# Kernel optimization log

Hardware: AMD Instinct MI355X
Metric: run time of the kernel (lower is better)

The kernel has to match this reference:

```python
import jax, jax.numpy as jnp
import numpy as np

N, DH, DK, FF = 2048, 256, 64, 32


def setup_inputs() -> dict:
    key = jax.random.key(0)
    ks = jax.random.split(key, 12)
    s = lambda d: 1.0 / np.sqrt(d).astype(np.float32)
    return {
        "x": jax.random.normal(ks[0], (1, N, DH), dtype=jnp.float32),
        "adj": (jax.random.uniform(ks[1], (N, N)) < 0.05).astype(jnp.float32),
        "dense": jax.random.uniform(ks[2], (N, N), dtype=jnp.float32),
        "Wq": jax.random.normal(ks[3], (DH, DK)) * s(DH),
        "bq": jnp.zeros((DK,), jnp.float32),
        "Wk": jax.random.normal(ks[4], (DH, DK)) * s(DH),
        "bk": jnp.zeros((DK,), jnp.float32),
        "Wv": jax.random.normal(ks[5], (DH, DH)) * s(DH),
        "bv": jnp.zeros((DH,), jnp.float32),
        "W1": jax.random.normal(ks[6], (3, FF)) * s(3),
        "b1": jnp.zeros((FF,), jnp.float32),
        "W2": jax.random.normal(ks[7], (FF, FF)) * s(FF),
        "b2": jnp.zeros((FF,), jnp.float32),
        "W3": jax.random.normal(ks[8], (FF, 1)) * s(FF),
        "b3": jnp.zeros((1,), jnp.float32),
    }


def reference(x, adj, dense, Wq, bq, Wk, bk, Wv, bv, W1, b1, W2, b2, W3, b3):
    # x: (1, n, dh). Original repeats x to (n, n, dh); here we exploit that
    # q[i, j] = Q(x_j), k[i, j] = K(x_i), v[i, j] = V(x_j) so no n^2*dh tensor
    # is materialized, while the math is identical.
    x0 = x[0]                      # (n, dh)
    q = x0 @ Wq + bq               # (n, dk), Q(x_j)
    k = x0 @ Wk + bk               # (n, dk), K(x_i)
    v = x0 @ Wv + bv               # (n, dh), V(x_j)
    # out[i, j] = <Q(x_j), K(x_i)>
    scores = k @ q.T               # (n, n)
    feats = jnp.stack((scores, adj, dense), axis=2)      # (n, n, 3)
    h = jax.nn.relu(feats @ W1 + b1)                     # (n, n, FF)
    h = jax.nn.relu(h @ W2 + b2)                         # (n, n, FF)
    focus = jax.nn.softmax((h @ W3 + b3)[..., 0], axis=1)  # (n, n)
    # feature[i] = sum_j focus[i, j] * V(x_j)
    feature = focus @ v            # (n, dh)
    return feature[None]           # (1, n, dh)
```

## Files before the change

kernel.cpp:

```cpp
#include <hip/hip_runtime.h>
#include <math.h>


#define NN  2048
#define DHH 256
#define DKK 64

typedef float    f32x4 __attribute__((ext_vector_type(4)));
typedef _Float16 f16x8 __attribute__((ext_vector_type(8)));
typedef _Float16 f16x4 __attribute__((ext_vector_type(4)));
typedef _Float16 f16x2 __attribute__((ext_vector_type(2)));

__global__ __launch_bounds__(256) void k_qkv(
    const float* __restrict__ x,
    const float* __restrict__ Wq, const float* __restrict__ bq,
    const float* __restrict__ Wk, const float* __restrict__ bk,
    const float* __restrict__ Wv, const float* __restrict__ bv,
    _Float16* __restrict__ q16, _Float16* __restrict__ k16,
    _Float16* __restrict__ vT)
{
    __shared__ float As[32][64];
    __shared__ float Bs[32][64];
    __shared__ _Float16 Ts[64 * 72];

    const int t  = threadIdx.x;
    const int m0 = blockIdx.x * 64;
    const int yb = blockIdx.y;

    const float* W; const float* bias; int wld; int cw0;
    if (yb == 0)      { W = Wq; bias = bq; wld = 64;  cw0 = 0; }
    else if (yb == 1) { W = Wk; bias = bk; wld = 64;  cw0 = 0; }
    else              { W = Wv; bias = bv; wld = 256; cw0 = (yb - 2) * 64; }

    const int tx = t & 15, ty = t >> 4;
    float acc[4][4] = {};

    for (int k0 = 0; k0 < DHH; k0 += 32) {
        {
            const int rr = t >> 3;
            const int cc = (t & 7) * 4;
            float4 a0 = *(const float4*)(x + (size_t)(m0 + rr)      * DHH + k0 + cc);
            float4 a1 = *(const float4*)(x + (size_t)(m0 + rr + 32) * DHH + k0 + cc);
            As[cc+0][rr]    = a0.x; As[cc+1][rr]    = a0.y; As[cc+2][rr]    = a0.z; As[cc+3][rr]    = a0.w;
            As[cc+0][rr+32] = a1.x; As[cc+1][rr+32] = a1.y; As[cc+2][rr+32] = a1.z; As[cc+3][rr+32] = a1.w;
        }
        {
            const int bk_ = t >> 4;
            const int bc  = (t & 15) * 4;
            *(float4*)&Bs[bk_][bc]      = *(const float4*)(W + (size_t)(k0 + bk_)      * wld + cw0 + bc);
            *(float4*)&Bs[bk_ + 16][bc] = *(const float4*)(W + (size_t)(k0 + bk_ + 16) * wld + cw0 + bc);
        }
        __syncthreads();
        #pragma unroll
        for (int kk = 0; kk < 32; ++kk) {
            float4 a = *(const float4*)&As[kk][ty * 4];
            float4 b = *(const float4*)&Bs[kk][tx * 4];
            float av[4] = {a.x, a.y, a.z, a.w};
            float bw[4] = {b.x, b.y, b.z, b.w};
            #pragma unroll
            for (int ii = 0; ii < 4; ++ii)
                #pragma unroll
                for (int jj = 0; jj < 4; ++jj)
                    acc[ii][jj] = fmaf(av[ii], bw[jj], acc[ii][jj]);
        }
        __syncthreads();
    }

    float4 b4 = *(const float4*)&bias[cw0 + tx * 4];
    float bc4[4] = {b4.x, b4.y, b4.z, b4.w};

    if (yb < 2) {
        _Float16* outp = (yb == 0) ? q16 : k16;
        #pragma unroll
        for (int ii = 0; ii < 4; ++ii) {
            f16x4 hv;
            #pragma unroll
            for (int jj = 0; jj < 4; ++jj) hv[jj] = (_Float16)(acc[ii][jj] + bc4[jj]);
            *(f16x4*)&outp[(size_t)(m0 + ty * 4 + ii) * 64 + tx * 4] = hv;
        }
    } else {
        #pragma unroll
        for (int jj = 0; jj < 4; ++jj) {
            f16x4 hv;
            #pragma unroll
            for (int ii = 0; ii < 4; ++ii) hv[ii] = (_Float16)(acc[ii][jj] + bc4[jj]);
            *(f16x4*)&Ts[(tx * 4 + jj) * 72 + ty * 4] = hv;
        }
        __syncthreads();
        {
            const int c = t >> 2, seg = t & 3;
            f16x8 r0 = *(const f16x8*)&Ts[c * 72 + seg * 16];
            f16x8 r1 = *(const f16x8*)&Ts[c * 72 + seg * 16 + 8];
            *(f16x8*)&vT[(size_t)(cw0 + c) * NN + m0 + seg * 16]     = r0;
            *(f16x8*)&vT[(size_t)(cw0 + c) * NN + m0 + seg * 16 + 8] = r1;
        }
    }
}

__global__ __launch_bounds__(256) void k_scores(
    const _Float16* __restrict__ q16, const _Float16* __restrict__ k16,
    _Float16* __restrict__ schi, _Float16* __restrict__ sclo)
{
    const int t    = threadIdx.x;
    const int lane = t & 63;
    const int w    = t >> 6;
    const int col  = lane & 15;
    const int q    = lane >> 4;

    const int i0 = blockIdx.y * 128 + (w >> 1) * 64;
    const int j0 = blockIdx.x * 128 + (w & 1) * 64;

    f32x4 acc[4][4] = {};

    #pragma unroll
    for (int ks = 0; ks < 2; ++ks) {
        f16x8 a[4], b[4];
        #pragma unroll
        for (int f = 0; f < 4; ++f) {
            a[f] = *(const f16x8*)&k16[(size_t)(i0 + f * 16 + col) * 64 + ks * 32 + q * 8];
            b[f] = *(const f16x8*)&q16[(size_t)(j0 + f * 16 + col) * 64 + ks * 32 + q * 8];
        }
        #pragma unroll
        for (int fm = 0; fm < 4; ++fm)
            #pragma unroll
            for (int fn = 0; fn < 4; ++fn)
                acc[fm][fn] = __builtin_amdgcn_mfma_f32_16x16x32_f16(a[fm], b[fn], acc[fm][fn], 0, 0, 0);
    }

    #pragma unroll
    for (int fm = 0; fm < 4; ++fm)
        #pragma unroll
        for (int fn = 0; fn < 4; ++fn)
            #pragma unroll
            for (int r = 0; r < 4; ++r) {
                const size_t idx = (size_t)(i0 + fm * 16 + q * 4 + r) * NN + j0 + fn * 16 + col;
                const float val = acc[fm][fn][r];
                const _Float16 h = (_Float16)val;
                schi[idx] = h;
                sclo[idx] = (_Float16)(val - (float)h);
            }
}

__global__ __launch_bounds__(256) void k_mlp(
    const _Float16* __restrict__ schi, const _Float16* __restrict__ sclo,
    const float* __restrict__ adj, const float* __restrict__ dense,
    const float* __restrict__ W1, const float* __restrict__ b1,
    const float* __restrict__ W2, const float* __restrict__ b2,
    const float* __restrict__ W3,
    _Float16* __restrict__ fhi)
{
    __shared__ _Float16 fA[4][64 * 8];
    __shared__ _Float16 hs[4][16 * 40];
    __shared__ _Float16 zsh[8];
    __shared__ float    lsg[NN];
    __shared__ float    red[8];

    const int t    = threadIdx.x;
    const int lane = t & 63;
    const int w    = t >> 6;
    const int col  = lane & 15;
    const int q    = lane >> 4;
    const int i    = blockIdx.x;

    if (t < 8) zsh[t] = (_Float16)0;
    __syncthreads();

    f16x8 w1f0 = {}, w1f1 = {};
    if (q == 0) {
        const int ne = 2 * col, no = 2 * col + 1;
        const float w0e = W1[0*32 + ne], w0o = W1[0*32 + no];
        const _Float16 w0eh = (_Float16)w0e, w0oh = (_Float16)w0o;
        w1f0[0] = w0eh; w1f0[1] = w0eh;
        w1f0[2] = (_Float16)W1[1*32 + ne];
        w1f0[3] = (_Float16)W1[2*32 + ne];
        w1f0[4] = (_Float16)(w0e - (float)w0eh);
        w1f1[0] = w0oh; w1f1[1] = w0oh;
        w1f1[2] = (_Float16)W1[1*32 + no];
        w1f1[3] = (_Float16)W1[2*32 + no];
        w1f1[4] = (_Float16)(w0o - (float)w0oh);
    }
    f16x8 w2f0, w2f1;
    #pragma unroll
    for (int j = 0; j < 8; ++j) {
        w2f0[j] = (_Float16)W2[(q * 8 + j) * 32 + col];
        w2f1[j] = (_Float16)W2[(q * 8 + j) * 32 + col + 16];
    }
    const float b1e = b1[2 * col], b1o = b1[2 * col + 1];
    const f32x4 c1e = {b1e, b1e, b1e, b1e};
    const f32x4 c1o = {b1o, b1o, b1o, b1o};
    f32x4 c2a, c2b, w3v, w3v2;
    #pragma unroll
    for (int r = 0; r < 4; ++r) {
        c2a[r]  = b2[q * 4 + r];
        c2b[r]  = b2[16 + q * 4 + r];
        w3v[r]  = W3[q * 4 + r];
        w3v2[r] = W3[16 + q * 4 + r];
    }

    const _Float16* shrow = schi + (size_t)i * NN;
    const _Float16* slrow = sclo + (size_t)i * NN;
    const float*    arow  = adj   + (size_t)i * NN;
    const float*    drow  = dense + (size_t)i * NN;

    for (int c = 0; c < 8; ++c) {
        const int base = w * 512 + c * 64;
        const int jj   = base + lane;

        {
            f16x8 fv = {shrow[jj], slrow[jj], (_Float16)arow[jj], (_Float16)drow[jj],
                        shrow[jj], (_Float16)0, (_Float16)0, (_Float16)0};
            *(f16x8*)&fA[w][lane * 8] = fv;
        }
        asm volatile("s_waitcnt lgkmcnt(0)" ::: "memory");

        #pragma unroll
        for (int st = 0; st < 4; ++st) {
            const _Float16* ap = (q == 0) ? &fA[w][(st * 16 + col) * 8] : zsh;
            f16x8 af = *(const f16x8*)ap;
            f32x4 hp0 = __builtin_amdgcn_mfma_f32_16x16x32_f16(af, w1f0, c1e, 0, 0, 0);
            f32x4 hp1 = __builtin_amdgcn_mfma_f32_16x16x32_f16(af, w1f1, c1o, 0, 0, 0);
            #pragma unroll
            for (int r = 0; r < 4; ++r) {
                f16x2 pk = __builtin_bit_cast(f16x2,
                    __builtin_amdgcn_cvt_pkrtz(fmaxf(hp0[r], 0.f), fmaxf(hp1[r], 0.f)));
                *(f16x2*)&hs[w][(q * 4 + r) * 40 + col * 2] = pk;
            }
            asm volatile("s_waitcnt lgkmcnt(0)" ::: "memory");

            f16x8 a2 = *(const f16x8*)&hs[w][col * 40 + q * 8];
            f32x4 acc0 = __builtin_amdgcn_mfma_f32_16x16x32_f16(w2f0, a2, c2a, 0, 0, 0);
            f32x4 acc1 = __builtin_amdgcn_mfma_f32_16x16x32_f16(w2f1, a2, c2b, 0, 0, 0);
            float p = 0.f;
            #pragma unroll
            for (int r = 0; r < 4; ++r) {
                p = fmaf(fmaxf(acc0[r], 0.f), w3v[r],  p);
                p = fmaf(fmaxf(acc1[r], 0.f), w3v2[r], p);
            }
            p += __shfl_xor(p, 16, 64);
            p += __shfl_xor(p, 32, 64);
            if (q == st) lsg[base + st * 16 + col] = p;
            asm volatile("s_waitcnt lgkmcnt(0)" ::: "memory");
        }
    }
    __syncthreads();

    float lv[8], lmax = -1e30f;
    #pragma unroll
    for (int u = 0; u < 8; ++u) { lv[u] = lsg[t + u * 256]; lmax = fmaxf(lmax, lv[u]); }
    #pragma unroll
    for (int off = 32; off > 0; off >>= 1)
        lmax = fmaxf(lmax, __shfl_xor(lmax, off, 64));
    if (lane == 0) red[w] = lmax;
    __syncthreads();
    const float rmax = fmaxf(fmaxf(red[0], red[1]), fmaxf(red[2], red[3]));

    float wgt[8], lsum = 0.f;
    #pragma unroll
    for (int u = 0; u < 8; ++u) { wgt[u] = __expf(lv[u] - rmax); lsum += wgt[u]; }
    #pragma unroll
    for (int off = 32; off > 0; off >>= 1)
        lsum += __shfl_xor(lsum, off, 64);
    if (lane == 0) red[4 + w] = lsum;
    __syncthreads();
    const float inv = 1.f / (red[4] + red[5] + red[6] + red[7]);

    _Float16* hrow = fhi + (size_t)i * NN;
    #pragma unroll
    for (int u = 0; u < 8; ++u)
        hrow[t + u * 256] = (_Float16)(wgt[u] * inv);
}

__global__ __launch_bounds__(256) void k_feat(
    const _Float16* __restrict__ fhi, const _Float16* __restrict__ vT,
    float* __restrict__ out)
{
    __shared__ float rbuf[3][64][8];

    const int t    = threadIdx.x;
    const int lane = t & 63;
    const int w    = t >> 6;
    const int col  = lane & 15;
    const int q    = lane >> 4;

    const int m0 = blockIdx.y * 16;
    const int n0 = blockIdx.x * 32;

    f32x4 acc0 = {}, acc1 = {};

    const size_t arow  = (size_t)(m0 + col) * NN;
    const size_t brow0 = (size_t)(n0 + col) * NN;
    const size_t brow1 = (size_t)(n0 + 16 + col) * NN;
    const int kb = w * 512 + q * 8;

    #pragma unroll 4
    for (int k0 = 0; k0 < 512; k0 += 32) {
        const int ko = kb + k0;
        f16x8 a  = *(const f16x8*)&fhi[arow + ko];
        f16x8 b0 = *(const f16x8*)&vT[brow0 + ko];
        f16x8 b1 = *(const f16x8*)&vT[brow1 + ko];
        acc0 = __builtin_amdgcn_mfma_f32_16x16x32_f16(a, b0, acc0, 0, 0, 0);
        acc1 = __builtin_amdgcn_mfma_f32_16x16x32_f16(a, b1, acc1, 0, 0, 0);
    }

    if (w != 0) {
        *(float4*)&rbuf[w - 1][lane][0] = *(float4*)&acc0;
        *(float4*)&rbuf[w - 1][lane][4] = *(float4*)&acc1;
    }
    __syncthreads();

    if (w == 0) {
        #pragma unroll
        for (int j = 0; j < 3; ++j) {
            float4 p0 = *(const float4*)&rbuf[j][lane][0];
            float4 p1 = *(const float4*)&rbuf[j][lane][4];
            acc0[0] += p0.x; acc0[1] += p0.y; acc0[2] += p0.z; acc0[3] += p0.w;
            acc1[0] += p1.x; acc1[1] += p1.y; acc1[2] += p1.z; acc1[3] += p1.w;
        }
        #pragma unroll
        for (int r = 0; r < 4; ++r) {
            out[(size_t)(m0 + q * 4 + r) * DHH + n0 + col]      = acc0[r];
            out[(size_t)(m0 + q * 4 + r) * DHH + n0 + 16 + col] = acc1[r];
        }
    }
}

extern "C" void kernel_launch(void* const* d_in, const int* in_sizes, int n_in,
                              void* d_out, int out_size, void* d_ws, size_t ws_size,
                              hipStream_t stream) {
    const float* x     = (const float*)d_in[0];
    const float* adj   = (const float*)d_in[1];
    const float* dense = (const float*)d_in[2];
    const float* Wq    = (const float*)d_in[3];
    const float* bq    = (const float*)d_in[4];
    const float* Wk    = (const float*)d_in[5];
    const float* bk    = (const float*)d_in[6];
    const float* Wv    = (const float*)d_in[7];
    const float* bv    = (const float*)d_in[8];
    const float* W1    = (const float*)d_in[9];
    const float* b1    = (const float*)d_in[10];
    const float* W2    = (const float*)d_in[11];
    const float* b2    = (const float*)d_in[12];
    const float* W3    = (const float*)d_in[13];
    float* out = (float*)d_out;

    char* wsb = (char*)d_ws;
    _Float16* q16  = (_Float16*)(wsb);
    _Float16* k16  = (_Float16*)(wsb + 262144);
    _Float16* vT   = (_Float16*)(wsb + 524288);
    _Float16* schi = (_Float16*)(wsb + 1572864);
    _Float16* sclo = (_Float16*)(wsb + 9961472);

    hipLaunchKernelGGL(k_qkv,    dim3(32, 6),  dim3(256), 0, stream,
                       x, Wq, bq, Wk, bk, Wv, bv, q16, k16, vT);
    hipLaunchKernelGGL(k_scores, dim3(16, 16), dim3(256), 0, stream, q16, k16, schi, sclo);
    hipLaunchKernelGGL(k_mlp,    dim3(2048),   dim3(256), 0, stream,
                       schi, sclo, adj, dense, W1, b1, W2, b2, W3, schi);
    hipLaunchKernelGGL(k_feat,   dim3(8, 128), dim3(256), 0, stream,
                       schi, vT, out);
}
```

Baseline: 183.8 us.

## Interleave score hi/lo halves and move MLP operand exchange from LDS to shuffles

The split-fp16 score is now stored as an interleaved hi/lo pair, so the MLP kernel reads one 4-byte word per element instead of two separate 2-byte streams. The MLP kernel drops its LDS staging buffers and barriers. It builds MFMA operands through cross-lane shuffles with transposed layer-1 roles, and keeps logits in registers instead of an LDS row buffer. The focus output overwrites the score buffer in place with a doubled row stride. This adds many shuffle instructions per step in place of the LDS round trips.

```diff
diff --git a/kernel.cpp b/kernel.cpp
--- a/kernel.cpp
+++ b/kernel.cpp
@@ -10,6 +10,7 @@
 typedef _Float16 f16x8 __attribute__((ext_vector_type(8)));
 typedef _Float16 f16x4 __attribute__((ext_vector_type(4)));
 typedef _Float16 f16x2 __attribute__((ext_vector_type(2)));
+typedef int      i32x4 __attribute__((ext_vector_type(4)));
 
 __global__ __launch_bounds__(256) void k_qkv(
     const float* __restrict__ x,
@@ -99,7 +100,7 @@
 
 __global__ __launch_bounds__(256) void k_scores(
     const _Float16* __restrict__ q16, const _Float16* __restrict__ k16,
-    _Float16* __restrict__ schi, _Float16* __restrict__ sclo)
+    f16x2* __restrict__ schl)
 {
     const int t    = threadIdx.x;
     const int lane = t & 63;
@@ -136,24 +137,20 @@
                 const size_t idx = (size_t)(i0 + fm * 16 + q * 4 + r) * NN + j0 + fn * 16 + col;
                 const float val = acc[fm][fn][r];
                 const _Float16 h = (_Float16)val;
-                schi[idx] = h;
-                sclo[idx] = (_Float16)(val - (float)h);
+                f16x2 pk; pk[0] = h; pk[1] = (_Float16)(val - (float)h);
+                schl[idx] = pk;
             }
 }
 
 __global__ __launch_bounds__(256) void k_mlp(
-    const _Float16* __restrict__ schi, const _Float16* __restrict__ sclo,
+    const f16x2* __restrict__ schl,
     const float* __restrict__ adj, const float* __restrict__ dense,
     const float* __restrict__ W1, const float* __restrict__ b1,
     const float* __restrict__ W2, const float* __restrict__ b2,
     const float* __restrict__ W3,
-    _Float16* __restrict__ fhi)
+    _Float16* __restrict__ focus)
 {
-    __shared__ _Float16 fA[4][64 * 8];
-    __shared__ _Float16 hs[4][16 * 40];
-    __shared__ _Float16 zsh[8];
-    __shared__ float    lsg[NN];
-    __shared__ float    red[8];
+    __shared__ float red[8];
 
     const int t    = threadIdx.x;
     const int lane = t & 63;
@@ -162,22 +159,18 @@
     const int q    = lane >> 4;
     const int i    = blockIdx.x;
 
-    if (t < 8) zsh[t] = (_Float16)0;
-    __syncthreads();
-
-    f16x8 w1f0 = {}, w1f1 = {};
+    f16x8 w1a0 = {}, w1a1 = {};
     if (q == 0) {
-        const int ne = 2 * col, no = 2 * col + 1;
-        const float w0e = W1[0*32 + ne], w0o = W1[0*32 + no];
-        const _Float16 w0eh = (_Float16)w0e, w0oh = (_Float16)w0o;
-        w1f0[0] = w0eh; w1f0[1] = w0eh;
-        w1f0[2] = (_Float16)W1[1*32 + ne];
-        w1f0[3] = (_Float16)W1[2*32 + ne];
-        w1f0[4] = (_Float16)(w0e - (float)w0eh);
-        w1f1[0] = w0oh; w1f1[1] = w0oh;
-        w1f1[2] = (_Float16)W1[1*32 + no];
-        w1f1[3] = (_Float16)W1[2*32 + no];
-        w1f1[4] = (_Float16)(w0o - (float)w0oh);
+        const float w0a = W1[col],      w0b = W1[col + 16];
+        const _Float16 h0a = (_Float16)w0a, h0b = (_Float16)w0b;
+        w1a0[0] = h0a; w1a0[1] = h0a;
+        w1a0[2] = (_Float16)W1[32 + col];
+        w1a0[3] = (_Float16)W1[64 + col];
+        w1a0[4] = (_Float16)(w0a - (float)h0a);
+        w1a1[0] = h0b; w1a1[1] = h0b;
+        w1a1[2] = (_Float16)W1[32 + col + 16];
+        w1a1[3] = (_Float16)W1[64 + col + 16];
+        w1a1[4] = (_Float16)(w0b - (float)h0b);
     }
     f16x8 w2f0, w2f1;
     #pragma unroll
@@ -185,51 +178,68 @@
         w2f0[j] = (_Float16)W2[(q * 8 + j) * 32 + col];
         w2f1[j] = (_Float16)W2[(q * 8 + j) * 32 + col + 16];
     }
-    const float b1e = b1[2 * col], b1o = b1[2 * col + 1];
-    const f32x4 c1e = {b1e, b1e, b1e, b1e};
-    const f32x4 c1o = {b1o, b1o, b1o, b1o};
-    f32x4 c2a, c2b, w3v, w3v2;
+    f32x4 c1a, c1b, c2a, c2b, w3v, w3v2;
     #pragma unroll
     for (int r = 0; r < 4; ++r) {
+        c1a[r]  = b1[q * 4 + r];
+        c1b[r]  = b1[16 + q * 4 + r];
         c2a[r]  = b2[q * 4 + r];
         c2b[r]  = b2[16 + q * 4 + r];
         w3v[r]  = W3[q * 4 + r];
         w3v2[r] = W3[16 + q * 4 + r];
     }
-
-    const _Float16* shrow = schi + (size_t)i * NN;
-    const _Float16* slrow = sclo + (size_t)i * NN;
-    const float*    arow  = adj   + (size_t)i * NN;
-    const float*    drow  = dense + (size_t)i * NN;
+    const int idxA = ((2 * q) & 3) * 16 + col;
+    const int idxB = ((2 * q + 1) & 3) * 16 + col;
+    const bool qlo = (q < 2);
+
+    const f16x2* srow = schl  + (size_t)i * NN;
+    const float* arow = adj   + (size_t)i * NN;
+    const float* drow = dense + (size_t)i * NN;
+
+    float lg[8];
 
     for (int c = 0; c < 8; ++c) {
-        const int base = w * 512 + c * 64;
-        const int jj   = base + lane;
-
-        {
-            f16x8 fv = {shrow[jj], slrow[jj], (_Float16)arow[jj], (_Float16)drow[jj],
-                        shrow[jj], (_Float16)0, (_Float16)0, (_Float16)0};
-            *(f16x8*)&fA[w][lane * 8] = fv;
-        }
-        asm volatile("s_waitcnt lgkmcnt(0)" ::: "memory");
-
+        const int jj = w * 512 + c * 64 + lane;
+
+        const int u_sa = __builtin_bit_cast(int, srow[jj]);
+        const int u_ad = __builtin_bit_cast(int,
+            __builtin_amdgcn_cvt_pkrtz(arow[jj], drow[jj]));
+        const int u_s0 = u_sa & 0xFFFF;
+
+        float lgc = 0.f;
         #pragma unroll
         for (int st = 0; st < 4; ++st) {
-            const _Float16* ap = (q == 0) ? &fA[w][(st * 16 + col) * 8] : zsh;
-            f16x8 af = *(const f16x8*)ap;
-            f32x4 hp0 = __builtin_amdgcn_mfma_f32_16x16x32_f16(af, w1f0, c1e, 0, 0, 0);
-            f32x4 hp1 = __builtin_amdgcn_mfma_f32_16x16x32_f16(af, w1f1, c1o, 0, 0, 0);
-            #pragma unroll
-            for (int r = 0; r < 4; ++r) {
-                f16x2 pk = __builtin_bit_cast(f16x2,
-                    __builtin_amdgcn_cvt_pkrtz(fmaxf(hp0[r], 0.f), fmaxf(hp1[r], 0.f)));
-                *(f16x2*)&hs[w][(q * 4 + r) * 40 + col * 2] = pk;
-            }
-            asm volatile("s_waitcnt lgkmcnt(0)" ::: "memory");
-
-            f16x8 a2 = *(const f16x8*)&hs[w][col * 40 + q * 8];
-            f32x4 acc0 = __builtin_amdgcn_mfma_f32_16x16x32_f16(w2f0, a2, c2a, 0, 0, 0);
-            f32x4 acc1 = __builtin_amdgcn_mfma_f32_16x16x32_f16(w2f1, a2, c2b, 0, 0, 0);
+            const int src = st * 16 + col;
+            int e0 = __shfl(u_sa, src, 64);
+            int e1 = __shfl(u_ad, src, 64);
+            int e2 = __shfl(u_s0, src, 64);
+            if (q != 0) { e0 = 0; e1 = 0; e2 = 0; }
+            i32x4 bv = {e0, e1, e2, 0};
+            f16x8 B1 = __builtin_bit_cast(f16x8, bv);
+
+            f32x4 hpA = __builtin_amdgcn_mfma_f32_16x16x32_f16(w1a0, B1, c1a, 0, 0, 0);
+            f32x4 hpB = __builtin_amdgcn_mfma_f32_16x16x32_f16(w1a1, B1, c1b, 0, 0, 0);
+
+            const int pA0 = __builtin_bit_cast(int, __builtin_amdgcn_cvt_pkrtz(fmaxf(hpA[0], 0.f), fmaxf(hpA[1], 0.f)));
+            const int pA1 = __builtin_bit_cast(int, __builtin_amdgcn_cvt_pkrtz(fmaxf(hpA[2], 0.f), fmaxf(hpA[3], 0.f)));
+            const int pB0 = __builtin_bit_cast(int, __builtin_amdgcn_cvt_pkrtz(fmaxf(hpB[0], 0.f), fmaxf(hpB[1], 0.f)));
+            const int pB1 = __builtin_bit_cast(int, __builtin_amdgcn_cvt_pkrtz(fmaxf(hpB[2], 0.f), fmaxf(hpB[3], 0.f)));
+
+            const int aA0 = __shfl(pA0, idxA, 64);
+            const int aA1 = __shfl(pA1, idxA, 64);
+            const int aB0 = __shfl(pB0, idxA, 64);
+            const int aB1 = __shfl(pB1, idxA, 64);
+            const int bA0 = __shfl(pA0, idxB, 64);
+            const int bA1 = __shfl(pA1, idxB, 64);
+            const int bB0 = __shfl(pB0, idxB, 64);
+            const int bB1 = __shfl(pB1, idxB, 64);
+            i32x4 b2v = { qlo ? aA0 : aB0, qlo ? aA1 : aB1,
+                          qlo ? bA0 : bB0, qlo ? bA1 : bB1 };
+            f16x8 B2 = __builtin_bit_cast(f16x8, b2v);
+
+            f32x4 acc0 = __builtin_amdgcn_mfma_f32_16x16x32_f16(w2f0, B2, c2a, 0, 0, 0);
+            f32x4 acc1 = __builtin_amdgcn_mfma_f32_16x16x32_f16(w2f1, B2, c2b, 0, 0, 0);
+
             float p = 0.f;
             #pragma unroll
             for (int r = 0; r < 4; ++r) {
@@ -238,15 +248,14 @@
             }
             p += __shfl_xor(p, 16, 64);
             p += __shfl_xor(p, 32, 64);
-            if (q == st) lsg[base + st * 16 + col] = p;
-            asm volatile("s_waitcnt lgkmcnt(0)" ::: "memory");
-        }
-    }
-    __syncthreads();
-
-    float lv[8], lmax = -1e30f;
-    #pragma unroll
-    for (int u = 0; u < 8; ++u) { lv[u] = lsg[t + u * 256]; lmax = fmaxf(lmax, lv[u]); }
+            lgc = (q == st) ? p : lgc;
+        }
+        lg[c] = lgc;
+    }
+
+    float lmax = -1e30f;
+    #pragma unroll
+    for (int u = 0; u < 8; ++u) lmax = fmaxf(lmax, lg[u]);
     #pragma unroll
     for (int off = 32; off > 0; off >>= 1)
         lmax = fmaxf(lmax, __shfl_xor(lmax, off, 64));
@@ -254,9 +263,9 @@
     __syncthreads();
     const float rmax = fmaxf(fmaxf(red[0], red[1]), fmaxf(red[2], red[3]));
 
-    float wgt[8], lsum = 0.f;
-    #pragma unroll
-    for (int u = 0; u < 8; ++u) { wgt[u] = __expf(lv[u] - rmax); lsum += wgt[u]; }
+    float lsum = 0.f;
+    #pragma unroll
+    for (int u = 0; u < 8; ++u) { lg[u] = __expf(lg[u] - rmax); lsum += lg[u]; }
     #pragma unroll
     for (int off = 32; off > 0; off >>= 1)
         lsum += __shfl_xor(lsum, off, 64);
@@ -264,14 +273,15 @@
     __syncthreads();
     const float inv = 1.f / (red[4] + red[5] + red[6] + red[7]);
 
-    _Float16* hrow = fhi + (size_t)i * NN;
+    _Float16* hrow = focus + (size_t)i * 2 * NN;
+    const int eb = w * 512 + q * 16 + col;
     #pragma unroll
     for (int u = 0; u < 8; ++u)
-        hrow[t + u * 256] = (_Float16)(wgt[u] * inv);
+        hrow[eb + u * 64] = (_Float16)(lg[u] * inv);
 }
 
 __global__ __launch_bounds__(256) void k_feat(
-    const _Float16* __restrict__ fhi, const _Float16* __restrict__ vT,
+    const _Float16* __restrict__ focus, const _Float16* __restrict__ vT,
     float* __restrict__ out)
 {
     __shared__ float rbuf[3][64][8];
@@ -287,7 +297,7 @@
 
     f32x4 acc0 = {}, acc1 = {};
 
-    const size_t arow  = (size_t)(m0 + col) * NN;
+    const size_t arow  = (size_t)(m0 + col) * (2 * NN);
     const size_t brow0 = (size_t)(n0 + col) * NN;
     const size_t brow1 = (size_t)(n0 + 16 + col) * NN;
     const int kb = w * 512 + q * 8;
@@ -295,7 +305,7 @@
     #pragma unroll 4
     for (int k0 = 0; k0 < 512; k0 += 32) {
         const int ko = kb + k0;
-        f16x8 a  = *(const f16x8*)&fhi[arow + ko];
+        f16x8 a  = *(const f16x8*)&focus[arow + ko];
         f16x8 b0 = *(const f16x8*)&vT[brow0 + ko];
         f16x8 b1 = *(const f16x8*)&vT[brow1 + ko];
         acc0 = __builtin_amdgcn_mfma_f32_16x16x32_f16(a, b0, acc0, 0, 0, 0);
@@ -347,14 +357,14 @@
     _Float16* q16  = (_Float16*)(wsb);
     _Float16* k16  = (_Float16*)(wsb + 262144);
     _Float16* vT   = (_Float16*)(wsb + 524288);
-    _Float16* schi = (_Float16*)(wsb + 1572864);
-    _Float16* sclo = (_Float16*)(wsb + 9961472);
+    f16x2*    schl = (f16x2*)   (wsb + 1572864);
+    _Float16* focus= (_Float16*)(wsb + 1572864);
 
     hipLaunchKernelGGL(k_qkv,    dim3(32, 6),  dim3(256), 0, stream,
                        x, Wq, bq, Wk, bk, Wv, bv, q16, k16, vT);
-    hipLaunchKernelGGL(k_scores, dim3(16, 16), dim3(256), 0, stream, q16, k16, schi, sclo);
+    hipLaunchKernelGGL(k_scores, dim3(16, 16), dim3(256), 0, stream, q16, k16, schl);
     hipLaunchKernelGGL(k_mlp,    dim3(2048),   dim3(256), 0, stream,
-                       schi, sclo, adj, dense, W1, b1, W2, b2, W3, schi);
+                       schl, adj, dense, W1, b1, W2, b2, W3, focus);
     hipLaunchKernelGGL(k_feat,   dim3(8, 128), dim3(256), 0, stream,
-                       schi, vT, out);
-}
+                       focus, vT, out);
+}
```

Measured after the change: 183.6 us. About the same (-0.1%).
